# Kernel tuning notes

Measured on AMD Instinct MI355X. Metric: run time of the kernel, lower is better.

The kernel has to match this reference:

```python
import jax, jax.numpy as jnp
import numpy as np

N = 100000   # nodes
E = 1600000  # edges
R = 8        # num_relations = 2 * n_speakers**2, n_speakers=2
G = 128      # g_dim
H1 = 64      # h1_dim
H2 = 64      # h2_dim (heads=1, concat)
NEG_SLOPE_ATT = 0.2   # RGATConv default negative_slope
NEG_SLOPE_OUT = 0.01  # F.leaky_relu default
BN_EPS = 1e-5


def setup_inputs() -> dict:
    key = jax.random.key(0)
    ks = jax.random.split(key, 13)
    node_features = jax.random.normal(ks[0], (N, G), dtype=jnp.float32)
    edge_index = jax.random.randint(ks[1], (2, E), 0, N, dtype=jnp.int64)
    edge_type = jax.random.randint(ks[2], (E,), 0, R, dtype=jnp.int64)
    # RGATConv layer 1: per-relation weight [R, in, heads*out], q/k [heads*out, heads], bias
    W1 = jax.random.normal(ks[3], (R, G, H1), dtype=jnp.float32) / np.float32(np.sqrt(G))
    q1 = jax.random.normal(ks[4], (H1, 1), dtype=jnp.float32) / np.float32(np.sqrt(H1))
    k1 = jax.random.normal(ks[5], (H1, 1), dtype=jnp.float32) / np.float32(np.sqrt(H1))
    b1 = jnp.zeros((H1,), dtype=jnp.float32)
    # RGATConv layer 2
    W2 = jax.random.normal(ks[6], (R, H1, H2), dtype=jnp.float32) / np.float32(np.sqrt(H1))
    q2 = jax.random.normal(ks[7], (H2, 1), dtype=jnp.float32) / np.float32(np.sqrt(H2))
    k2 = jax.random.normal(ks[8], (H2, 1), dtype=jnp.float32) / np.float32(np.sqrt(H2))
    b2 = jnp.zeros((H2,), dtype=jnp.float32)
    # BatchNorm1d affine params
    gamma = jnp.ones((H2,), dtype=jnp.float32)
    beta = jnp.zeros((H2,), dtype=jnp.float32)
    return {"node_features": node_features, "edge_index": edge_index,
            "edge_type": edge_type, "W1": W1, "q1": q1, "k1": k1, "b1": b1,
            "W2": W2, "q2": q2, "k2": k2, "b2": b2, "gamma": gamma, "beta": beta}


def _rgat_conv(x, src, dst, edge_type, W, q, k, b):
    # Per-relation dense transform for all nodes: [R, N, O] (R is small = 8)
    xw = jnp.einsum('ni,rio->rno', x, W)
    # Per-edge transformed endpoint features (gathered by relation + node id)
    hi = xw[edge_type, dst]   # [E, O] target-side
    hj = xw[edge_type, src]   # [E, O] source-side (message content)
    # Additive self-attention, across-relation softmax over incoming edges of dst
    alpha = jax.nn.leaky_relu(hi @ q + hj @ k, NEG_SLOPE_ATT)  # [E, 1]
    n = x.shape[0]
    m = jax.ops.segment_max(alpha, dst, num_segments=n)
    m = jnp.where(jnp.isfinite(m), m, 0.0)  # nodes with no in-edges
    e = jnp.exp(alpha - m[dst])
    denom = jax.ops.segment_sum(e, dst, num_segments=n)
    a = e / (denom[dst] + 1e-16)
    # Weighted scatter-add aggregation (heads=1, concat)
    out = jax.ops.segment_sum(hj * a, dst, num_segments=n)  # [N, O]
    return out + b


def reference(node_features, edge_index, edge_type, W1, q1, k1, b1,
              W2, q2, k2, b2, gamma, beta):
    src = edge_index[0]  # source j (messages flow src -> dst)
    dst = edge_index[1]  # target i
    x = _rgat_conv(node_features, src, dst, edge_type, W1, q1, k1, b1)
    x = jax.nn.relu(x)
    x = _rgat_conv(x, src, dst, edge_type, W2, q2, k2, b2)
    # BatchNorm1d (training-mode batch statistics, biased variance)
    mean = jnp.mean(x, axis=0)
    var = jnp.var(x, axis=0)
    x = (x - mean) * jax.lax.rsqrt(var + BN_EPS) * gamma + beta
    return jax.nn.leaky_relu(x, NEG_SLOPE_OUT)
```

## Files before the change

### kernel.cpp

```cpp
#include <hip/hip_runtime.h>
#include <hip/hip_bf16.h>

#define NN 100000
#define EE 1600000
#define RR 8
#define NBKT 196
#define ACHUNK 8192

typedef __attribute__((ext_vector_type(8))) short bf16x8;
typedef __attribute__((ext_vector_type(4))) float f32x4;

__device__ __forceinline__ unsigned short f2bf(float v) {
    __hip_bfloat16 h = __float2bfloat16(v);
    return *reinterpret_cast<unsigned short*>(&h);
}
__device__ __forceinline__ float bf2f(unsigned short u) {
    unsigned x = (unsigned)u << 16;
    return __uint_as_float(x);
}
__device__ __forceinline__ unsigned fmap(float a) {
    unsigned u = __float_as_uint(a);
    return (u & 0x80000000u) ? ~u : (u | 0x80000000u);
}
__device__ __forceinline__ float funmap(unsigned u) {
    return (u & 0x80000000u) ? __uint_as_float(u & 0x7FFFFFFFu) : __uint_as_float(~u);
}

template<int IN_DIM>
__global__ __launch_bounds__(256)
void wt_frag(const float* __restrict__ W, unsigned short* __restrict__ Wf) {
    constexpr int KSTEPS = IN_DIM / 32;
    int r = blockIdx.x;
    for (int i = threadIdx.x; i < IN_DIM * 64; i += 256) {
        int k = i >> 6, o = i & 63;
        int ks = k >> 5, quad = (k >> 3) & 3, j = k & 7;
        int tl = o >> 4, l16 = o & 15;
        int lane = quad * 16 + l16;
        size_t idx = ((((size_t)r * KSTEPS + ks) * 4 + tl) * 64 + lane) * 8 + j;
        Wf[idx] = f2bf(W[((size_t)r * IN_DIM + k) * 64 + o]);
    }
}

template<int IN_DIM>
__global__ __launch_bounds__(256)
void wqk_frag(const float* __restrict__ W, const float* __restrict__ q,
              const float* __restrict__ k, unsigned short* __restrict__ Sf) {
    for (int i = blockIdx.x * 256 + threadIdx.x; i < IN_DIM * 16; i += gridDim.x * 256) {
        int j = i & 7, lane = (i >> 3) & 63, ks = i >> 9;
        int col = lane & 15, quad = lane >> 4;
        int kd = ks * 32 + quad * 8 + j;
        const float* v = (col < 8) ? q : k;
        int r = (col < 8) ? col : col - 8;
        float s = 0.f;
        #pragma unroll
        for (int o = 0; o < 64; o++) s += W[((size_t)r * IN_DIM + kd) * 64 + o] * v[o];
        Sf[i] = f2bf(s);
    }
}

__global__ void init_mxk16(unsigned* __restrict__ a, unsigned* __restrict__ b) {
    if (threadIdx.x < RR) { a[threadIdx.x] = fmap(-1e30f); b[threadIdx.x] = fmap(-1e30f); }
}

__global__ __launch_bounds__(256)
void sk_max(const float* __restrict__ sk, unsigned* __restrict__ mxk_u) {
    int r = blockIdx.x;
    int t = threadIdx.x;
    float m = -1e30f;
    for (int i = blockIdx.y * (NN / 8) + t; i < (blockIdx.y + 1) * (NN / 8); i += 256)
        m = fmaxf(m, sk[(size_t)r * NN + i]);
    #pragma unroll
    for (int off = 32; off >= 1; off >>= 1)
        m = fmaxf(m, __shfl_xor(m, off, 64));
    __shared__ float sm[4];
    if ((t & 63) == 0) sm[t >> 6] = m;
    __syncthreads();
    if (t == 0) {
        m = fmaxf(fmaxf(sm[0], sm[1]), fmaxf(sm[2], sm[3]));
        atomicMax(&mxk_u[r], fmap(m));
    }
}

template<int IN_DIM>
__global__ __launch_bounds__(256)
void gemm_mfma(const float* __restrict__ x, const unsigned short* __restrict__ Wf,
               const unsigned short* __restrict__ Sf,
               unsigned short* __restrict__ xw,
               float* __restrict__ sq, float* __restrict__ sk)
{
    constexpr int KSTEPS = IN_DIM / 32;
    constexpr int NB = IN_DIM / 8;
    __shared__ unsigned short xl[64 * IN_DIM];

    const int n0 = blockIdx.x * 64;
    const int t = threadIdx.x;
    const int wave = t >> 6, lane = t & 63;
    const int quad = lane >> 4, l16 = lane & 15;

    for (int c = t; c < 64 * IN_DIM / 4; c += 256) {
        int row = c / (IN_DIM / 4), kc = (c % (IN_DIM / 4)) * 4;
        float4 v = make_float4(0.f, 0.f, 0.f, 0.f);
        int gr = n0 + row;
        if (gr < NN) v = *(const float4*)(x + (size_t)gr * IN_DIM + kc);
        ushort4 u;
        u.x = f2bf(v.x); u.y = f2bf(v.y); u.z = f2bf(v.z); u.w = f2bf(v.w);
        int b = kc >> 3;
        *(ushort4*)&xl[row * IN_DIM + ((b ^ (row & (NB - 1))) << 3) + (kc & 7)] = u;
    }
    __syncthreads();

    bf16x8 afr[KSTEPS];
    const int arow = wave * 16 + l16;
    #pragma unroll
    for (int ks = 0; ks < KSTEPS; ks++) {
        int b = ks * 4 + quad;
        afr[ks] = *(const bf16x8*)&xl[arow * IN_DIM + ((b ^ (arow & (NB - 1))) << 3)];
    }

    {
        f32x4 accs = {0.f, 0.f, 0.f, 0.f};
        #pragma unroll
        for (int ks = 0; ks < KSTEPS; ks++) {
            bf16x8 sfr = *(const bf16x8*)&Sf[(ks * 64 + lane) * 8];
            accs = __builtin_amdgcn_mfma_f32_16x16x32_bf16(afr[ks], sfr, accs, 0, 0, 0);
        }
        #pragma unroll
        for (int reg = 0; reg < 4; reg++) {
            int grow = n0 + wave * 16 + quad * 4 + reg;
            if (grow < NN) {
                if (l16 < 8) sq[(size_t)l16 * NN + grow] = accs[reg];
                else         sk[(size_t)(l16 - 8) * NN + grow] = accs[reg];
            }
        }
    }

    #pragma unroll 1
    for (int r = 0; r < RR; r++) {
        bf16x8 bfr[KSTEPS][4];
        const unsigned short* Wb = Wf + (((size_t)r * KSTEPS) * 4) * 64 * 8 + lane * 8;
        #pragma unroll
        for (int ks = 0; ks < KSTEPS; ks++)
            #pragma unroll
            for (int tl = 0; tl < 4; tl++)
                bfr[ks][tl] = *(const bf16x8*)(Wb + ((ks * 4 + tl) * 64) * 8);

        f32x4 acc[4] = {{0.f,0.f,0.f,0.f},{0.f,0.f,0.f,0.f},{0.f,0.f,0.f,0.f},{0.f,0.f,0.f,0.f}};
        #pragma unroll
        for (int ks = 0; ks < KSTEPS; ks++)
            #pragma unroll
            for (int tl = 0; tl < 4; tl++)
                acc[tl] = __builtin_amdgcn_mfma_f32_16x16x32_bf16(afr[ks], bfr[ks][tl], acc[tl], 0, 0, 0);

        const size_t rbase = (size_t)r * NN;
        #pragma unroll
        for (int reg = 0; reg < 4; reg++) {
            int grow = n0 + wave * 16 + quad * 4 + reg;
            if (grow < NN) {
                ushort4 u;
                u.x = f2bf(acc[0][reg]); u.y = f2bf(acc[1][reg]);
                u.z = f2bf(acc[2][reg]); u.w = f2bf(acc[3][reg]);
                *(ushort4*)(xw + (rbase + grow) * 64 + l16 * 4) = u;
            }
        }
    }
}

__global__ __launch_bounds__(256)
void bucket_hist(const int* __restrict__ dst, unsigned* __restrict__ bcnt) {
    __shared__ unsigned h[NBKT];
    int t = threadIdx.x;
    for (int i = t; i < NBKT; i += 256) h[i] = 0;
    __syncthreads();
    int e0 = blockIdx.x * ACHUNK;
    for (int i = t; i < ACHUNK; i += 256) {
        int e = e0 + i;
        if (e < EE) atomicAdd(&h[((unsigned)dst[e]) >> 9], 1u);
    }
    __syncthreads();
    for (int i = t; i < NBKT; i += 256)
        if (h[i]) atomicAdd(&bcnt[i], h[i]);
}

__global__ void bucket_scan(const unsigned* __restrict__ bcnt, unsigned* __restrict__ bstart,
                            unsigned* __restrict__ bcur, unsigned* __restrict__ rowstart) {
    if (threadIdx.x == 0) {
        unsigned run = 0;
        for (int i = 0; i < NBKT; i++) { bstart[i] = run; bcur[i] = run; run += bcnt[i]; }
        bstart[NBKT] = run;
        rowstart[NN] = EE;
    }
}

__global__ __launch_bounds__(256)
void part_scatter(const int* __restrict__ src, const int* __restrict__ dst,
                  const int* __restrict__ et, unsigned* __restrict__ bcur,
                  unsigned* __restrict__ tmp) {
    __shared__ unsigned h[NBKT], base[NBKT];
    int t = threadIdx.x;
    for (int i = t; i < NBKT; i += 256) h[i] = 0;
    __syncthreads();
    int e0 = blockIdx.x * ACHUNK;
    for (int i = t; i < ACHUNK; i += 256) {
        int e = e0 + i;
        if (e < EE) atomicAdd(&h[((unsigned)dst[e]) >> 9], 1u);
    }
    __syncthreads();
    for (int i = t; i < NBKT; i += 256) {
        base[i] = h[i] ? atomicAdd(&bcur[i], h[i]) : 0u;
        h[i] = 0;
    }
    __syncthreads();
    for (int i = t; i < ACHUNK; i += 256) {
        int e = e0 + i;
        if (e < EE) {
            unsigned d = (unsigned)dst[e];
            unsigned b = d >> 9;
            unsigned off = atomicAdd(&h[b], 1u);
            unsigned val = ((d & 511u) << 23) | ((unsigned)et[e] << 20) | (unsigned)src[e];
            tmp[base[b] + off] = val;
        }
    }
}

__global__ __launch_bounds__(512)
void bucket_csr(const unsigned* __restrict__ bstart, const unsigned* __restrict__ tmp,
                unsigned* __restrict__ rowstart, unsigned* __restrict__ pk) {
    __shared__ unsigned lcnt[512], lscan[512], lrs[512];
    int b = blockIdx.x, t = threadIdx.x;
    unsigned ebeg = bstart[b], eend = bstart[b + 1];
    lcnt[t] = 0;
    __syncthreads();
    for (unsigned i = ebeg + t; i < eend; i += 512)
        atomicAdd(&lcnt[tmp[i] >> 23], 1u);
    __syncthreads();
    unsigned v = lcnt[t];
    lscan[t] = v;
    __syncthreads();
    for (int off = 1; off < 512; off <<= 1) {
        unsigned u = (t >= off) ? lscan[t - off] : 0u;
        __syncthreads();
        lscan[t] += u;
        __syncthreads();
    }
    unsigned excl = lscan[t] - v;
    lrs[t] = ebeg + excl;
    int node = b * 512 + t;
    if (node < NN) rowstart[node] = ebeg + excl;
    lcnt[t] = 0;
    __syncthreads();
    for (unsigned i = ebeg + t; i < eend; i += 512) {
        unsigned val = tmp[i];
        unsigned d = val >> 23;
        unsigned pos = lrs[d] + atomicAdd(&lcnt[d], 1u);
        pk[pos] = val & 0x7FFFFFu;
    }
}

template<int LAYER>
__global__ __launch_bounds__(256)
void node_aggregate(const unsigned* __restrict__ rowstart, const unsigned* __restrict__ pk,
                    const float* __restrict__ sq, const float* __restrict__ sk,
                    const unsigned* __restrict__ mxk_u,
                    const unsigned short* __restrict__ xw, const float* __restrict__ b,
                    float* __restrict__ out)
{
    int node = blockIdx.x * 4 + (threadIdx.x >> 6);
    int lane = threadIdx.x & 63;
    int g = lane >> 4, c16 = lane & 15;
    unsigned beg = rowstart[node], end = rowstart[node + 1];

    float sqv[RR];
    float m = -1e30f;
    #pragma unroll
    for (int r = 0; r < RR; r++) {
        sqv[r] = sq[(size_t)r * NN + node];
        m = fmaxf(m, sqv[r] + funmap(mxk_u[r]));
    }
    m = m > 0.f ? m : 0.2f * m;

    float a0 = 0.f, a1 = 0.f, a2 = 0.f, a3 = 0.f, den = 0.f;
    for (unsigned c0 = beg; c0 < end; c0 += 64) {
        unsigned i = c0 + lane;
        float w = 0.f;
        unsigned rowidx = 0;
        if (i < end) {
            unsigned p = pk[i];
            unsigned r = p >> 20;
            rowidx = r * NN + (p & 0xFFFFFu);
            float a = sqv[r] + sk[rowidx];
            a = a > 0.f ? a : 0.2f * a;
            w = __expf(a - m);
            den += w;
        }
        int cnt4 = ((int)min(64u, end - c0) + 3) & ~3;
        for (int j = 0; j < cnt4; j += 4) {
            float    wj = __shfl(w, j + g, 64);
            unsigned rj = (unsigned)__shfl((int)rowidx, j + g, 64);
            ushort4 v4 = *(const ushort4*)(xw + (size_t)rj * 64 + c16 * 4);
            a0 += wj * bf2f(v4.x);
            a1 += wj * bf2f(v4.y);
            a2 += wj * bf2f(v4.z);
            a3 += wj * bf2f(v4.w);
        }
    }
    #pragma unroll
    for (int off = 32; off >= 1; off >>= 1)
        den += __shfl_xor(den, off, 64);
    a0 += __shfl_xor(a0, 16, 64); a0 += __shfl_xor(a0, 32, 64);
    a1 += __shfl_xor(a1, 16, 64); a1 += __shfl_xor(a1, 32, 64);
    a2 += __shfl_xor(a2, 16, 64); a2 += __shfl_xor(a2, 32, 64);
    a3 += __shfl_xor(a3, 16, 64); a3 += __shfl_xor(a3, 32, 64);

    float accg = (g == 0) ? a0 : (g == 1) ? a1 : (g == 2) ? a2 : a3;
    float res = (end > beg) ? accg / (den + 1e-16f) : 0.f;
    int c = g * 16 + c16;
    if constexpr (LAYER == 1) {
        res += b[c];
        res = res > 0.f ? res : 0.f;
    }
    out[(size_t)node * 64 + c] = res;
}

__global__ __launch_bounds__(256)
void bn_stats(const float* __restrict__ x, float* __restrict__ stats)
{
    int c = threadIdx.x & 63;
    int w = threadIdx.x >> 6;
    float s = 0.f, s2 = 0.f;
    for (int row = blockIdx.x * 4 + w; row < NN; row += gridDim.x * 4) {
        float v = x[(size_t)row * 64 + c];
        s += v; s2 += v * v;
    }
    __shared__ float ls[4][64], ls2[4][64];
    ls[w][c] = s; ls2[w][c] = s2;
    __syncthreads();
    if (threadIdx.x < 64) {
        atomicAdd(&stats[c],      ls[0][c] + ls[1][c] + ls[2][c] + ls[3][c]);
        atomicAdd(&stats[64 + c], ls2[0][c] + ls2[1][c] + ls2[2][c] + ls2[3][c]);
    }
}

__global__ __launch_bounds__(256)
void bn_apply(float* __restrict__ x, const float* __restrict__ stats,
              const float* __restrict__ gamma, const float* __restrict__ beta)
{
    int i = blockIdx.x * 256 + threadIdx.x;
    if (i >= NN * 64) return;
    int c = i & 63;
    float mean = stats[c] * (1.f / NN);
    float var  = stats[64 + c] * (1.f / NN) - mean * mean;
    float sc   = rsqrtf(var + 1e-5f) * gamma[c];
    float v = (x[i] - mean) * sc + beta[c];
    x[i] = v > 0.f ? v : 0.01f * v;
}

extern "C" void kernel_launch(void* const* d_in, const int* in_sizes, int n_in,
                              void* d_out, int out_size, void* d_ws, size_t ws_size,
                              hipStream_t stream)
{
    const float* x0 = (const float*)d_in[0];
    const int*   ei = (const int*)d_in[1];
    const int*   et = (const int*)d_in[2];
    const float* W1 = (const float*)d_in[3];
    const float* q1 = (const float*)d_in[4];
    const float* k1 = (const float*)d_in[5];
    const float* b1 = (const float*)d_in[6];
    const float* W2 = (const float*)d_in[7];
    const float* q2 = (const float*)d_in[8];
    const float* k2 = (const float*)d_in[9];
    const float* gamma = (const float*)d_in[11];
    const float* beta  = (const float*)d_in[12];
    const int* src = ei;
    const int* dst = ei + EE;
    float* out = (float*)d_out;

    char* base = (char*)d_ws;
    size_t off = 0;
    auto take = [&](size_t bytes) -> char* {
        char* p = base + off;
        off = (off + bytes + 255) & ~(size_t)255;
        return p;
    };
    float*    sq       = (float*)take((size_t)RR * NN * 4);
    float*    sk       = (float*)take((size_t)RR * NN * 4);
    unsigned* rowstart = (unsigned*)take((size_t)(NN + 1) * 4);
    unsigned* bcnt     = (unsigned*)take((size_t)NBKT * 4);
    unsigned* bstart   = (unsigned*)take((size_t)(NBKT + 1) * 4);
    unsigned* bcur     = (unsigned*)take((size_t)NBKT * 4);
    unsigned* tmp      = (unsigned*)take((size_t)EE * 4);
    unsigned* pk       = (unsigned*)take((size_t)EE * 4);
    float*    x1       = (float*)take((size_t)NN * 64 * 4);
    float*    stats    = (float*)take(512);
    unsigned* mxk1     = (unsigned*)take(RR * 4);
    unsigned* mxk2     = (unsigned*)take(RR * 4);
    unsigned short* Wf1 = (unsigned short*)take((size_t)RR * 64 * 128 * 2);
    unsigned short* Wf2 = (unsigned short*)take((size_t)RR * 64 * 64 * 2);
    unsigned short* Sf1 = (unsigned short*)take((size_t)128 * 16 * 2);
    unsigned short* Sf2 = (unsigned short*)take((size_t)64 * 16 * 2);
    unsigned short* xw  = (unsigned short*)take((size_t)RR * NN * 64 * 2);

    const int nb_nodes = (NN + 63) / 64;
    const int nb_part  = (EE + ACHUNK - 1) / ACHUNK;
    const int nb_agg   = NN / 4;
    const int nb_elem  = (NN * 64) / 256;

    wt_frag<128><<<RR, 256, 0, stream>>>(W1, Wf1);
    wt_frag<64><<<RR, 256, 0, stream>>>(W2, Wf2);
    wqk_frag<128><<<8, 256, 0, stream>>>(W1, q1, k1, Sf1);
    wqk_frag<64><<<4, 256, 0, stream>>>(W2, q2, k2, Sf2);
    init_mxk16<<<1, 64, 0, stream>>>(mxk1, mxk2);

    hipMemsetAsync(bcnt, 0, (size_t)NBKT * 4, stream);
    bucket_hist<<<nb_part, 256, 0, stream>>>(dst, bcnt);
    bucket_scan<<<1, 64, 0, stream>>>(bcnt, bstart, bcur, rowstart);
    part_scatter<<<nb_part, 256, 0, stream>>>(src, dst, et, bcur, tmp);
    bucket_csr<<<NBKT, 512, 0, stream>>>(bstart, tmp, rowstart, pk);

    gemm_mfma<128><<<nb_nodes, 256, 0, stream>>>(x0, Wf1, Sf1, xw, sq, sk);
    sk_max<<<dim3(RR, 8), 256, 0, stream>>>(sk, mxk1);
    node_aggregate<1><<<nb_agg, 256, 0, stream>>>(rowstart, pk, sq, sk, mxk1, xw, b1, x1);

    gemm_mfma<64><<<nb_nodes, 256, 0, stream>>>(x1, Wf2, Sf2, xw, sq, sk);
    sk_max<<<dim3(RR, 8), 256, 0, stream>>>(sk, mxk2);
    node_aggregate<2><<<nb_agg, 256, 0, stream>>>(rowstart, pk, sq, sk, mxk2, xw, nullptr, out);

    hipMemsetAsync(stats, 0, 2 * 64 * 4, stream);
    bn_stats<<<512, 256, 0, stream>>>(out, stats);
    bn_apply<<<nb_elem, 256, 0, stream>>>(out, stats, gamma, beta);
}
```

Measured before the change: 486.2 us.

## Fuse prep kernels, bucket with fixed capacity, fold max and BN stats into producers

```diff
diff --git a/kernel.cpp b/kernel.cpp
--- a/kernel.cpp
+++ b/kernel.cpp
@@ -6,6 +6,7 @@
 #define RR 8
 #define NBKT 196
 #define ACHUNK 8192
+#define CAP 10240
 
 typedef __attribute__((ext_vector_type(8))) short bf16x8;
 typedef __attribute__((ext_vector_type(4))) float f32x4;
@@ -27,10 +28,9 @@
 }
 
 template<int IN_DIM>
-__global__ __launch_bounds__(256)
-void wt_frag(const float* __restrict__ W, unsigned short* __restrict__ Wf) {
+__device__ __forceinline__ void wt_frag_dev(const float* __restrict__ W,
+                                            unsigned short* __restrict__ Wf, int r) {
     constexpr int KSTEPS = IN_DIM / 32;
-    int r = blockIdx.x;
     for (int i = threadIdx.x; i < IN_DIM * 64; i += 256) {
         int k = i >> 6, o = i & 63;
         int ks = k >> 5, quad = (k >> 3) & 3, j = k & 7;
@@ -42,10 +42,10 @@
 }
 
 template<int IN_DIM>
-__global__ __launch_bounds__(256)
-void wqk_frag(const float* __restrict__ W, const float* __restrict__ q,
-              const float* __restrict__ k, unsigned short* __restrict__ Sf) {
-    for (int i = blockIdx.x * 256 + threadIdx.x; i < IN_DIM * 16; i += gridDim.x * 256) {
+__device__ __forceinline__ void wqk_frag_dev(const float* __restrict__ W,
+        const float* __restrict__ q, const float* __restrict__ k,
+        unsigned short* __restrict__ Sf, int blk, int nb) {
+    for (int i = blk * 256 + threadIdx.x; i < IN_DIM * 16; i += nb * 256) {
         int j = i & 7, lane = (i >> 3) & 63, ks = i >> 9;
         int col = lane & 15, quad = lane >> 4;
         int kd = ks * 32 + quad * 8 + j;
@@ -58,39 +58,110 @@
     }
 }
 
-__global__ void init_mxk16(unsigned* __restrict__ a, unsigned* __restrict__ b) {
-    if (threadIdx.x < RR) { a[threadIdx.x] = fmap(-1e30f); b[threadIdx.x] = fmap(-1e30f); }
-}
-
 __global__ __launch_bounds__(256)
-void sk_max(const float* __restrict__ sk, unsigned* __restrict__ mxk_u) {
-    int r = blockIdx.x;
+void prep(const float* __restrict__ W1, const float* __restrict__ q1, const float* __restrict__ k1,
+          const float* __restrict__ W2, const float* __restrict__ q2, const float* __restrict__ k2,
+          unsigned short* __restrict__ Wf1, unsigned short* __restrict__ Wf2,
+          unsigned short* __restrict__ Sf1, unsigned short* __restrict__ Sf2,
+          unsigned* __restrict__ mxk1, unsigned* __restrict__ mxk2,
+          unsigned* __restrict__ bcnt, float* __restrict__ stats)
+{
+    int b = blockIdx.x;
+    if (b < 8)        wt_frag_dev<128>(W1, Wf1, b);
+    else if (b < 16)  wt_frag_dev<64>(W2, Wf2, b - 8);
+    else if (b < 20)  wqk_frag_dev<128>(W1, q1, k1, Sf1, b - 16, 4);
+    else if (b == 20) wqk_frag_dev<64>(W2, q2, k2, Sf2, 0, 1);
+    else {
+        int t = threadIdx.x;
+        if (t < RR) { mxk1[t] = fmap(-1e30f); mxk2[t] = fmap(-1e30f); }
+        if (t < NBKT) bcnt[t] = 0;
+        if (t < 128) stats[t] = 0.f;
+    }
+}
+
+__global__ __launch_bounds__(256)
+void part_scatter(const int* __restrict__ src, const int* __restrict__ dst,
+                  const int* __restrict__ et, unsigned* __restrict__ bcnt,
+                  unsigned* __restrict__ tmp) {
+    __shared__ unsigned h[NBKT], base[NBKT];
     int t = threadIdx.x;
-    float m = -1e30f;
-    for (int i = blockIdx.y * (NN / 8) + t; i < (blockIdx.y + 1) * (NN / 8); i += 256)
-        m = fmaxf(m, sk[(size_t)r * NN + i]);
-    #pragma unroll
-    for (int off = 32; off >= 1; off >>= 1)
-        m = fmaxf(m, __shfl_xor(m, off, 64));
-    __shared__ float sm[4];
-    if ((t & 63) == 0) sm[t >> 6] = m;
-    __syncthreads();
-    if (t == 0) {
-        m = fmaxf(fmaxf(sm[0], sm[1]), fmaxf(sm[2], sm[3]));
-        atomicMax(&mxk_u[r], fmap(m));
-    }
-}
-
-template<int IN_DIM>
+    for (int i = t; i < NBKT; i += 256) h[i] = 0;
+    __syncthreads();
+    int e0 = blockIdx.x * ACHUNK;
+    for (int i = t; i < ACHUNK; i += 256) {
+        int e = e0 + i;
+        if (e < EE) atomicAdd(&h[((unsigned)dst[e]) >> 9], 1u);
+    }
+    __syncthreads();
+    for (int i = t; i < NBKT; i += 256) {
+        base[i] = (unsigned)i * CAP + (h[i] ? atomicAdd(&bcnt[i], h[i]) : 0u);
+        h[i] = 0;
+    }
+    __syncthreads();
+    for (int i = t; i < ACHUNK; i += 256) {
+        int e = e0 + i;
+        if (e < EE) {
+            unsigned d = (unsigned)dst[e];
+            unsigned bk = d >> 9;
+            unsigned off = atomicAdd(&h[bk], 1u);
+            unsigned pos = base[bk] + off;
+            if (pos < (bk + 1u) * CAP) {
+                unsigned val = ((d & 511u) << 23) | ((unsigned)et[e] << 20) | (unsigned)src[e];
+                tmp[pos] = val;
+            }
+        }
+    }
+}
+
+__global__ __launch_bounds__(512)
+void bucket_csr(const unsigned* __restrict__ bcnt, const unsigned* __restrict__ tmp,
+                unsigned* __restrict__ rowstart, unsigned* __restrict__ rowdeg,
+                unsigned* __restrict__ pk) {
+    __shared__ unsigned lcnt[512], lscan[512], lrs[512];
+    int b = blockIdx.x, t = threadIdx.x;
+    unsigned ebeg = (unsigned)b * CAP;
+    unsigned cnt = min(bcnt[b], (unsigned)CAP);
+    unsigned eend = ebeg + cnt;
+    lcnt[t] = 0;
+    __syncthreads();
+    for (unsigned i = ebeg + t; i < eend; i += 512)
+        atomicAdd(&lcnt[tmp[i] >> 23], 1u);
+    __syncthreads();
+    unsigned v = lcnt[t];
+    lscan[t] = v;
+    __syncthreads();
+    for (int off = 1; off < 512; off <<= 1) {
+        unsigned u = (t >= off) ? lscan[t - off] : 0u;
+        __syncthreads();
+        lscan[t] += u;
+        __syncthreads();
+    }
+    unsigned excl = lscan[t] - v;
+    lrs[t] = ebeg + excl;
+    int node = b * 512 + t;
+    if (node < NN) { rowstart[node] = ebeg + excl; rowdeg[node] = v; }
+    lcnt[t] = 0;
+    __syncthreads();
+    for (unsigned i = ebeg + t; i < eend; i += 512) {
+        unsigned val = tmp[i];
+        unsigned d = val >> 23;
+        unsigned pos = lrs[d] + atomicAdd(&lcnt[d], 1u);
+        pk[pos] = val & 0x7FFFFFu;
+    }
+}
+
+template<int IN_DIM, bool BF16IN>
 __global__ __launch_bounds__(256)
-void gemm_mfma(const float* __restrict__ x, const unsigned short* __restrict__ Wf,
+void gemm_mfma(const void* __restrict__ xv, const unsigned short* __restrict__ Wf,
                const unsigned short* __restrict__ Sf,
                unsigned short* __restrict__ xw,
-               float* __restrict__ sq, float* __restrict__ sk)
+               float* __restrict__ sq, float* __restrict__ sk,
+               unsigned* __restrict__ mxk)
 {
     constexpr int KSTEPS = IN_DIM / 32;
     constexpr int NB = IN_DIM / 8;
     __shared__ unsigned short xl[64 * IN_DIM];
+    __shared__ float smax[4][8];
 
     const int n0 = blockIdx.x * 64;
     const int t = threadIdx.x;
@@ -99,11 +170,16 @@
 
     for (int c = t; c < 64 * IN_DIM / 4; c += 256) {
         int row = c / (IN_DIM / 4), kc = (c % (IN_DIM / 4)) * 4;
-        float4 v = make_float4(0.f, 0.f, 0.f, 0.f);
         int gr = n0 + row;
-        if (gr < NN) v = *(const float4*)(x + (size_t)gr * IN_DIM + kc);
-        ushort4 u;
-        u.x = f2bf(v.x); u.y = f2bf(v.y); u.z = f2bf(v.z); u.w = f2bf(v.w);
+        ushort4 u = make_ushort4(0, 0, 0, 0);
+        if constexpr (BF16IN) {
+            if (gr < NN) u = *(const ushort4*)((const unsigned short*)xv + (size_t)gr * IN_DIM + kc);
+        } else {
+            if (gr < NN) {
+                float4 v = *(const float4*)((const float*)xv + (size_t)gr * IN_DIM + kc);
+                u.x = f2bf(v.x); u.y = f2bf(v.y); u.z = f2bf(v.z); u.w = f2bf(v.w);
+            }
+        }
         int b = kc >> 3;
         *(ushort4*)&xl[row * IN_DIM + ((b ^ (row & (NB - 1))) << 3) + (kc & 7)] = u;
     }
@@ -124,14 +200,23 @@
             bf16x8 sfr = *(const bf16x8*)&Sf[(ks * 64 + lane) * 8];
             accs = __builtin_amdgcn_mfma_f32_16x16x32_bf16(afr[ks], sfr, accs, 0, 0, 0);
         }
+        float pm = -1e30f;
         #pragma unroll
         for (int reg = 0; reg < 4; reg++) {
             int grow = n0 + wave * 16 + quad * 4 + reg;
             if (grow < NN) {
                 if (l16 < 8) sq[(size_t)l16 * NN + grow] = accs[reg];
-                else         sk[(size_t)(l16 - 8) * NN + grow] = accs[reg];
+                else { sk[(size_t)(l16 - 8) * NN + grow] = accs[reg]; pm = fmaxf(pm, accs[reg]); }
             }
         }
+        pm = fmaxf(pm, __shfl_xor(pm, 16, 64));
+        pm = fmaxf(pm, __shfl_xor(pm, 32, 64));
+        if (quad == 0 && l16 >= 8) smax[wave][l16 - 8] = pm;
+    }
+    __syncthreads();
+    if (t < 8) {
+        float v = fmaxf(fmaxf(smax[0][t], smax[1][t]), fmaxf(smax[2][t], smax[3][t]));
+        atomicMax(&mxk[t], fmap(v));
     }
 
     #pragma unroll 1
@@ -165,143 +250,61 @@
     }
 }
 
-__global__ __launch_bounds__(256)
-void bucket_hist(const int* __restrict__ dst, unsigned* __restrict__ bcnt) {
-    __shared__ unsigned h[NBKT];
-    int t = threadIdx.x;
-    for (int i = t; i < NBKT; i += 256) h[i] = 0;
-    __syncthreads();
-    int e0 = blockIdx.x * ACHUNK;
-    for (int i = t; i < ACHUNK; i += 256) {
-        int e = e0 + i;
-        if (e < EE) atomicAdd(&h[((unsigned)dst[e]) >> 9], 1u);
-    }
-    __syncthreads();
-    for (int i = t; i < NBKT; i += 256)
-        if (h[i]) atomicAdd(&bcnt[i], h[i]);
-}
-
-__global__ void bucket_scan(const unsigned* __restrict__ bcnt, unsigned* __restrict__ bstart,
-                            unsigned* __restrict__ bcur, unsigned* __restrict__ rowstart) {
-    if (threadIdx.x == 0) {
-        unsigned run = 0;
-        for (int i = 0; i < NBKT; i++) { bstart[i] = run; bcur[i] = run; run += bcnt[i]; }
-        bstart[NBKT] = run;
-        rowstart[NN] = EE;
-    }
-}
-
-__global__ __launch_bounds__(256)
-void part_scatter(const int* __restrict__ src, const int* __restrict__ dst,
-                  const int* __restrict__ et, unsigned* __restrict__ bcur,
-                  unsigned* __restrict__ tmp) {
-    __shared__ unsigned h[NBKT], base[NBKT];
-    int t = threadIdx.x;
-    for (int i = t; i < NBKT; i += 256) h[i] = 0;
-    __syncthreads();
-    int e0 = blockIdx.x * ACHUNK;
-    for (int i = t; i < ACHUNK; i += 256) {
-        int e = e0 + i;
-        if (e < EE) atomicAdd(&h[((unsigned)dst[e]) >> 9], 1u);
-    }
-    __syncthreads();
-    for (int i = t; i < NBKT; i += 256) {
-        base[i] = h[i] ? atomicAdd(&bcur[i], h[i]) : 0u;
-        h[i] = 0;
-    }
-    __syncthreads();
-    for (int i = t; i < ACHUNK; i += 256) {
-        int e = e0 + i;
-        if (e < EE) {
-            unsigned d = (unsigned)dst[e];
-            unsigned b = d >> 9;
-            unsigned off = atomicAdd(&h[b], 1u);
-            unsigned val = ((d & 511u) << 23) | ((unsigned)et[e] << 20) | (unsigned)src[e];
-            tmp[base[b] + off] = val;
-        }
-    }
-}
-
-__global__ __launch_bounds__(512)
-void bucket_csr(const unsigned* __restrict__ bstart, const unsigned* __restrict__ tmp,
-                unsigned* __restrict__ rowstart, unsigned* __restrict__ pk) {
-    __shared__ unsigned lcnt[512], lscan[512], lrs[512];
-    int b = blockIdx.x, t = threadIdx.x;
-    unsigned ebeg = bstart[b], eend = bstart[b + 1];
-    lcnt[t] = 0;
-    __syncthreads();
-    for (unsigned i = ebeg + t; i < eend; i += 512)
-        atomicAdd(&lcnt[tmp[i] >> 23], 1u);
-    __syncthreads();
-    unsigned v = lcnt[t];
-    lscan[t] = v;
-    __syncthreads();
-    for (int off = 1; off < 512; off <<= 1) {
-        unsigned u = (t >= off) ? lscan[t - off] : 0u;
-        __syncthreads();
-        lscan[t] += u;
-        __syncthreads();
-    }
-    unsigned excl = lscan[t] - v;
-    lrs[t] = ebeg + excl;
-    int node = b * 512 + t;
-    if (node < NN) rowstart[node] = ebeg + excl;
-    lcnt[t] = 0;
-    __syncthreads();
-    for (unsigned i = ebeg + t; i < eend; i += 512) {
-        unsigned val = tmp[i];
-        unsigned d = val >> 23;
-        unsigned pos = lrs[d] + atomicAdd(&lcnt[d], 1u);
-        pk[pos] = val & 0x7FFFFFu;
-    }
-}
-
 template<int LAYER>
 __global__ __launch_bounds__(256)
-void node_aggregate(const unsigned* __restrict__ rowstart, const unsigned* __restrict__ pk,
+void node_aggregate(const unsigned* __restrict__ rowstart, const unsigned* __restrict__ rowdeg,
+                    const unsigned* __restrict__ pk,
                     const float* __restrict__ sq, const float* __restrict__ sk,
                     const unsigned* __restrict__ mxk_u,
                     const unsigned short* __restrict__ xw, const float* __restrict__ b,
-                    float* __restrict__ out)
+                    void* __restrict__ outv, float* __restrict__ stats)
 {
-    int node = blockIdx.x * 4 + (threadIdx.x >> 6);
-    int lane = threadIdx.x & 63;
-    int g = lane >> 4, c16 = lane & 15;
-    unsigned beg = rowstart[node], end = rowstart[node + 1];
-
-    float sqv[RR];
-    float m = -1e30f;
-    #pragma unroll
-    for (int r = 0; r < RR; r++) {
-        sqv[r] = sq[(size_t)r * NN + node];
-        m = fmaxf(m, sqv[r] + funmap(mxk_u[r]));
-    }
-    m = m > 0.f ? m : 0.2f * m;
+    __shared__ float2 ew[4][64];
+    __shared__ float bs[4][64], bs2[4][64];
+    const int wv = threadIdx.x >> 6;
+    const int node = blockIdx.x * 4 + wv;
+    const int lane = threadIdx.x & 63;
+    const int g = lane >> 4, c16 = lane & 15;
+    const unsigned beg = rowstart[node];
+    const unsigned deg = rowdeg[node];
+    const unsigned end = beg + deg;
+
+    const float sqreg = sq[(size_t)(lane & 7) * NN + node];
+    float tmx = sqreg + funmap(mxk_u[lane & 7]);
+    tmx = fmaxf(tmx, __shfl_xor(tmx, 1, 64));
+    tmx = fmaxf(tmx, __shfl_xor(tmx, 2, 64));
+    tmx = fmaxf(tmx, __shfl_xor(tmx, 4, 64));
+    const float m = tmx > 0.f ? tmx : 0.2f * tmx;
 
     float a0 = 0.f, a1 = 0.f, a2 = 0.f, a3 = 0.f, den = 0.f;
+    float2* ews = ew[wv];
     for (unsigned c0 = beg; c0 < end; c0 += 64) {
         unsigned i = c0 + lane;
-        float w = 0.f;
-        unsigned rowidx = 0;
-        if (i < end) {
-            unsigned p = pk[i];
-            unsigned r = p >> 20;
-            rowidx = r * NN + (p & 0xFFFFFu);
-            float a = sqv[r] + sk[rowidx];
-            a = a > 0.f ? a : 0.2f * a;
-            w = __expf(a - m);
-            den += w;
-        }
-        int cnt4 = ((int)min(64u, end - c0) + 3) & ~3;
-        for (int j = 0; j < cnt4; j += 4) {
-            float    wj = __shfl(w, j + g, 64);
-            unsigned rj = (unsigned)__shfl((int)rowidx, j + g, 64);
-            ushort4 v4 = *(const ushort4*)(xw + (size_t)rj * 64 + c16 * 4);
-            a0 += wj * bf2f(v4.x);
-            a1 += wj * bf2f(v4.y);
-            a2 += wj * bf2f(v4.z);
-            a3 += wj * bf2f(v4.w);
-        }
+        unsigned p = 0;
+        if (i < end) p = pk[i];
+        unsigned r = p >> 20;
+        unsigned rowidx = r * NN + (p & 0xFFFFFu);
+        float skv = sk[rowidx];
+        float sqv_e = __shfl(sqreg, (int)r, 64);
+        float a = sqv_e + skv;
+        a = a > 0.f ? a : 0.2f * a;
+        float w = __expf(a - m);
+        if (i >= end) w = 0.f;
+        den += w;
+        ews[lane] = make_float2(w, __uint_as_float(rowidx));
+        __builtin_amdgcn_wave_barrier();
+        int cnt8 = ((int)min(64u, end - c0) + 7) & ~7;
+        for (int j = 0; j < cnt8; j += 8) {
+            float2 e0 = ews[j + g];
+            float2 e1 = ews[j + 4 + g];
+            ushort4 v0 = *(const ushort4*)(xw + (size_t)__float_as_uint(e0.y) * 64 + c16 * 4);
+            ushort4 v1 = *(const ushort4*)(xw + (size_t)__float_as_uint(e1.y) * 64 + c16 * 4);
+            a0 += e0.x * bf2f(v0.x) + e1.x * bf2f(v1.x);
+            a1 += e0.x * bf2f(v0.y) + e1.x * bf2f(v1.y);
+            a2 += e0.x * bf2f(v0.z) + e1.x * bf2f(v1.z);
+            a3 += e0.x * bf2f(v0.w) + e1.x * bf2f(v1.w);
+        }
+        __builtin_amdgcn_wave_barrier();
     }
     #pragma unroll
     for (int off = 32; off >= 1; off >>= 1)
@@ -312,31 +315,24 @@
     a3 += __shfl_xor(a3, 16, 64); a3 += __shfl_xor(a3, 32, 64);
 
     float accg = (g == 0) ? a0 : (g == 1) ? a1 : (g == 2) ? a2 : a3;
-    float res = (end > beg) ? accg / (den + 1e-16f) : 0.f;
+    float res = (deg > 0) ? accg / (den + 1e-16f) : 0.f;
     int c = g * 16 + c16;
     if constexpr (LAYER == 1) {
         res += b[c];
         res = res > 0.f ? res : 0.f;
-    }
-    out[(size_t)node * 64 + c] = res;
-}
-
-__global__ __launch_bounds__(256)
-void bn_stats(const float* __restrict__ x, float* __restrict__ stats)
-{
-    int c = threadIdx.x & 63;
-    int w = threadIdx.x >> 6;
-    float s = 0.f, s2 = 0.f;
-    for (int row = blockIdx.x * 4 + w; row < NN; row += gridDim.x * 4) {
-        float v = x[(size_t)row * 64 + c];
-        s += v; s2 += v * v;
-    }
-    __shared__ float ls[4][64], ls2[4][64];
-    ls[w][c] = s; ls2[w][c] = s2;
-    __syncthreads();
-    if (threadIdx.x < 64) {
-        atomicAdd(&stats[c],      ls[0][c] + ls[1][c] + ls[2][c] + ls[3][c]);
-        atomicAdd(&stats[64 + c], ls2[0][c] + ls2[1][c] + ls2[2][c] + ls2[3][c]);
+        ((unsigned short*)outv)[(size_t)node * 64 + c] = f2bf(res);
+    } else {
+        ((float*)outv)[(size_t)node * 64 + c] = res;
+        bs[wv][c] = res;
+        bs2[wv][c] = res * res;
+        __syncthreads();
+        int t = threadIdx.x;
+        if (t < 64) {
+            float s  = bs[0][t] + bs[1][t] + bs[2][t] + bs[3][t];
+            float s2 = bs2[0][t] + bs2[1][t] + bs2[2][t] + bs2[3][t];
+            atomicAdd(&stats[t], s);
+            atomicAdd(&stats[64 + t], s2);
+        }
     }
 }
 
@@ -383,17 +379,16 @@
     };
     float*    sq       = (float*)take((size_t)RR * NN * 4);
     float*    sk       = (float*)take((size_t)RR * NN * 4);
-    unsigned* rowstart = (unsigned*)take((size_t)(NN + 1) * 4);
+    unsigned* rowstart = (unsigned*)take((size_t)NN * 4);
+    unsigned* rowdeg   = (unsigned*)take((size_t)NN * 4);
     unsigned* bcnt     = (unsigned*)take((size_t)NBKT * 4);
-    unsigned* bstart   = (unsigned*)take((size_t)(NBKT + 1) * 4);
-    unsigned* bcur     = (unsigned*)take((size_t)NBKT * 4);
-    unsigned* tmp      = (unsigned*)take((size_t)EE * 4);
-    unsigned* pk       = (unsigned*)take((size_t)EE * 4);
-    float*    x1       = (float*)take((size_t)NN * 64 * 4);
+    unsigned* tmp      = (unsigned*)take((size_t)NBKT * CAP * 4);
+    unsigned* pk       = (unsigned*)take((size_t)NBKT * CAP * 4);
+    unsigned short* x1 = (unsigned short*)take((size_t)NN * 64 * 2);
     float*    stats    = (float*)take(512);
     unsigned* mxk1     = (unsigned*)take(RR * 4);
     unsigned* mxk2     = (unsigned*)take(RR * 4);
-    unsigned short* Wf1 = (unsigned short*)take((size_t)RR * 64 * 128 * 2);
+    unsigned short* Wf1 = (unsigned short*)take((size_t)RR * 128 * 64 * 2);
     unsigned short* Wf2 = (unsigned short*)take((size_t)RR * 64 * 64 * 2);
     unsigned short* Sf1 = (unsigned short*)take((size_t)128 * 16 * 2);
     unsigned short* Sf2 = (unsigned short*)take((size_t)64 * 16 * 2);
@@ -404,27 +399,18 @@
     const int nb_agg   = NN / 4;
     const int nb_elem  = (NN * 64) / 256;
 
-    wt_frag<128><<<RR, 256, 0, stream>>>(W1, Wf1);
-    wt_frag<64><<<RR, 256, 0, stream>>>(W2, Wf2);
-    wqk_frag<128><<<8, 256, 0, stream>>>(W1, q1, k1, Sf1);
-    wqk_frag<64><<<4, 256, 0, stream>>>(W2, q2, k2, Sf2);
-    init_mxk16<<<1, 64, 0, stream>>>(mxk1, mxk2);
-
-    hipMemsetAsync(bcnt, 0, (size_t)NBKT * 4, stream);
-    bucket_hist<<<nb_part, 256, 0, stream>>>(dst, bcnt);
-    bucket_scan<<<1, 64, 0, stream>>>(bcnt, bstart, bcur, rowstart);
-    part_scatter<<<nb_part, 256, 0, stream>>>(src, dst, et, bcur, tmp);
-    bucket_csr<<<NBKT, 512, 0, stream>>>(bstart, tmp, rowstart, pk);
-
-    gemm_mfma<128><<<nb_nodes, 256, 0, stream>>>(x0, Wf1, Sf1, xw, sq, sk);
-    sk_max<<<dim3(RR, 8), 256, 0, stream>>>(sk, mxk1);
-    node_aggregate<1><<<nb_agg, 256, 0, stream>>>(rowstart, pk, sq, sk, mxk1, xw, b1, x1);
-
-    gemm_mfma<64><<<nb_nodes, 256, 0, stream>>>(x1, Wf2, Sf2, xw, sq, sk);
-    sk_max<<<dim3(RR, 8), 256, 0, stream>>>(sk, mxk2);
-    node_aggregate<2><<<nb_agg, 256, 0, stream>>>(rowstart, pk, sq, sk, mxk2, xw, nullptr, out);
-
-    hipMemsetAsync(stats, 0, 2 * 64 * 4, stream);
-    bn_stats<<<512, 256, 0, stream>>>(out, stats);
+    prep<<<22, 256, 0, stream>>>(W1, q1, k1, W2, q2, k2, Wf1, Wf2, Sf1, Sf2,
+                                 mxk1, mxk2, bcnt, stats);
+    part_scatter<<<nb_part, 256, 0, stream>>>(src, dst, et, bcnt, tmp);
+    bucket_csr<<<NBKT, 512, 0, stream>>>(bcnt, tmp, rowstart, rowdeg, pk);
+
+    gemm_mfma<128, false><<<nb_nodes, 256, 0, stream>>>(x0, Wf1, Sf1, xw, sq, sk, mxk1);
+    node_aggregate<1><<<nb_agg, 256, 0, stream>>>(rowstart, rowdeg, pk, sq, sk, mxk1,
+                                                  xw, b1, x1, nullptr);
+
+    gemm_mfma<64, true><<<nb_nodes, 256, 0, stream>>>(x1, Wf2, Sf2, xw, sq, sk, mxk2);
+    node_aggregate<2><<<nb_agg, 256, 0, stream>>>(rowstart, rowdeg, pk, sq, sk, mxk2,
+                                                  xw, nullptr, out, stats);
+
     bn_apply<<<nb_elem, 256, 0, stream>>>(out, stats, gamma, beta);
 }
```

Result: slower. 963.6 us (+98.2%).
